# Kernel tuning notes

Hardware: AMD Instinct MI355X
Metric: run time of the kernel (lower is better)

The kernel has to match this reference:

```python
import jax, jax.numpy as jnp
import numpy as np

N_NODES = 25000
N_EDGES = 400000
D_FEAT = 64      # 2 * per-endpoint feature dim (concat of both endpoints)
STATE_DIM = 16
OUT_DIM = 16
MAX_IT = 5
THRESHOLD = 0.01


def setup_inputs() -> dict:
    key = jax.random.key(0)
    ks = jax.random.split(key, 8)
    edge_src = jax.random.randint(ks[0], (N_EDGES,), 0, N_NODES)
    edge_dst = jax.random.randint(ks[1], (N_EDGES,), 0, N_NODES)
    edge_feat = jax.random.normal(ks[2], (N_EDGES, D_FEAT), jnp.float32)
    w = lambda k, s: jax.random.normal(k, s, jnp.float32) * 0.1
    return {
        "edge_feat": edge_feat,
        "Wst1": w(ks[3], (D_FEAT + STATE_DIM, 2 * STATE_DIM)),
        "bst1": jnp.zeros((2 * STATE_DIM,), jnp.float32),
        "Wst2": w(ks[4], (2 * STATE_DIM, STATE_DIM)),
        "bst2": jnp.zeros((STATE_DIM,), jnp.float32),
        "Wout1": w(ks[5], (STATE_DIM, 2 * STATE_DIM)),
        "bout1": jnp.zeros((2 * STATE_DIM,), jnp.float32),
        "Wout2": w(ks[6], (2 * STATE_DIM, OUT_DIM)),
        "bout2": jnp.zeros((OUT_DIM,), jnp.float32),
        "edge_src": edge_src,
        "edge_dst": edge_dst,
        "n_nodes": N_NODES,
    }


def reference(edge_feat, Wst1, bst1, Wst2, bst2, Wout1, bout1, Wout2, bout2,
              edge_src, edge_dst, n_nodes):
    s = Wst2.shape[1]
    state0 = jnp.zeros((n_nodes, s), edge_feat.dtype)

    def step(carry, _):
        state, done = carry
        gat = state[edge_dst]                                   # [E, s] gather
        x = jnp.concatenate([edge_feat, gat], axis=1)           # [E, 2d+s]
        res = jnp.tanh(jnp.tanh(x @ Wst1 + bst1) @ Wst2 + bst2)  # state MLP
        new_state = jax.ops.segment_sum(res, edge_src, num_segments=n_nodes)
        # per-node L2 change; stop (freeze) once all nodes are below threshold
        dist = jnp.sqrt(jnp.sum((new_state - state) ** 2, axis=1) + 1e-10)
        converged = jnp.all(dist <= THRESHOLD)
        state = jnp.where(done, state, new_state)
        return (state, done | converged), None

    (state, _), _ = jax.lax.scan(step, (state0, jnp.array(False)), None, length=MAX_IT)
    h = jnp.tanh(state @ Wout1 + bout1)
    out = jax.nn.softmax(h @ Wout2 + bout2, axis=-1)  # [n_nodes, out_dim]
    return out
```

## Files before the change

### kernel.cpp

```cpp
#include <hip/hip_runtime.h>
#include <cstddef>

#define D_FEAT 64
#define S_DIM 16
#define H_DIM 32
#define OUT_DIM 16
#define MAX_IT 5

typedef _Float16 half8 __attribute__((ext_vector_type(8)));

__device__ __forceinline__ float fast_tanh(float x) {
    float xc = fminf(fmaxf(x, -15.0f), 15.0f);
    float e = __expf(2.0f * xc);
    return (e - 1.0f) / (e + 1.0f);
}

__global__ __launch_bounds__(256)
void k_hist(const int* __restrict__ src, int* __restrict__ deg, int E) {
    int e = blockIdx.x * 256 + threadIdx.x;
    if (e < E) atomicAdd(&deg[src[e]], 1);
}

__global__ __launch_bounds__(1024)
void k_scan(const int* __restrict__ deg, int* __restrict__ cursor, int N) {
    __shared__ int wsum[16];
    __shared__ int carry;
    int lane = threadIdx.x & 63;
    int wid = threadIdx.x >> 6;
    if (threadIdx.x == 0) carry = 0;
    __syncthreads();
    for (int base = 0; base < N; base += 1024) {
        int i = base + (int)threadIdx.x;
        int v = (i < N) ? deg[i] : 0;
        int incl = v;
#pragma unroll
        for (int off = 1; off < 64; off <<= 1) {
            int t = __shfl_up(incl, off, 64);
            if (lane >= off) incl += t;
        }
        if (lane == 63) wsum[wid] = incl;
        __syncthreads();
        if (wid == 0) {
            int w = (lane < 16) ? wsum[lane] : 0;
            int wi = w;
#pragma unroll
            for (int off = 1; off < 16; off <<= 1) {
                int t = __shfl_up(wi, off, 64);
                if (lane >= off) wi += t;
            }
            if (lane < 16) wsum[lane] = wi - w;
        }
        __syncthreads();
        int excl = incl - v + wsum[wid] + carry;
        if (i < N) cursor[i] = excl;
        __syncthreads();
        if ((int)threadIdx.x == 1023) carry = excl + v;
        __syncthreads();
    }
}

__global__ __launch_bounds__(256)
void k_scatter(const int* __restrict__ src, const int* __restrict__ dst,
               int* __restrict__ cursor, int* __restrict__ pos,
               int* __restrict__ dstp, int* __restrict__ srcp, int E) {
    int e = blockIdx.x * 256 + threadIdx.x;
    if (e >= E) return;
    int s = src[e];
    int p = atomicAdd(&cursor[s], 1);
    pos[e] = p;
    dstp[p] = dst[e];
    srcp[p] = s;
}

__global__ __launch_bounds__(256)
void k_pre(const float* __restrict__ feat, const float* __restrict__ Wst1,
           const float* __restrict__ bst1, const int* __restrict__ pos,
           _Float16* __restrict__ pre, int E) {
    int e = blockIdx.x * 256 + threadIdx.x;
    if (e >= E) return;
    float acc[H_DIM];
#pragma unroll
    for (int j = 0; j < H_DIM; ++j) acc[j] = bst1[j];
    const float4* f4 = reinterpret_cast<const float4*>(feat + (size_t)e * D_FEAT);
#pragma unroll 4
    for (int k4 = 0; k4 < D_FEAT / 4; ++k4) {
        float4 v = f4[k4];
        const float* w = Wst1 + k4 * 4 * H_DIM;
#pragma unroll
        for (int j = 0; j < H_DIM; ++j) acc[j] = fmaf(v.x, w[j], acc[j]);
#pragma unroll
        for (int j = 0; j < H_DIM; ++j) acc[j] = fmaf(v.y, w[H_DIM + j], acc[j]);
#pragma unroll
        for (int j = 0; j < H_DIM; ++j) acc[j] = fmaf(v.z, w[2 * H_DIM + j], acc[j]);
#pragma unroll
        for (int j = 0; j < H_DIM; ++j) acc[j] = fmaf(v.w, w[3 * H_DIM + j], acc[j]);
    }
    int p = pos[e];
    half8* op = reinterpret_cast<half8*>(pre + (size_t)p * H_DIM);
#pragma unroll
    for (int j8 = 0; j8 < 4; ++j8) {
        half8 v;
#pragma unroll
        for (int k = 0; k < 8; ++k) v[k] = (_Float16)acc[j8 * 8 + k];
        op[j8] = v;
    }
}

__global__ __launch_bounds__(256)
void k_edge(const _Float16* __restrict__ pre, const float* __restrict__ nodeH,
            const int* __restrict__ dstp, const int* __restrict__ srcp,
            const float* __restrict__ Wst2, const float* __restrict__ bst2,
            float* __restrict__ new_state, const int* __restrict__ flags,
            int it, int E) {
#pragma unroll
    for (int j = 0; j < MAX_IT; ++j)
        if (j < it && flags[2 + j] == 0) return;
    __shared__ float sres[256][17];
    __shared__ int ssrc[256];
    __shared__ int send[256];
    __shared__ int segs[256];
    __shared__ int wf[4];
    __shared__ int nseg;
    const int t = threadIdx.x;
    const int lane = t & 63;
    const int wid = t >> 6;
    const int base = blockIdx.x * 256;
    const int ep = base + t;
    const bool valid = ep < E;
    if (t == 0) nseg = 0;

    int s = valid ? srcp[ep] : (int)0x80000000;
    ssrc[t] = s;

    if (valid) {
        int d = dstp[ep];
        const half8* pp = reinterpret_cast<const half8*>(pre + (size_t)ep * H_DIM);
        const float4* hp = reinterpret_cast<const float4*>(nodeH + (size_t)d * H_DIM);
        float h[H_DIM];
#pragma unroll
        for (int j8 = 0; j8 < 4; ++j8) {
            half8 pv = pp[j8];
            float4 a = hp[j8 * 2], b = hp[j8 * 2 + 1];
            h[j8 * 8 + 0] = fast_tanh((float)pv[0] + a.x);
            h[j8 * 8 + 1] = fast_tanh((float)pv[1] + a.y);
            h[j8 * 8 + 2] = fast_tanh((float)pv[2] + a.z);
            h[j8 * 8 + 3] = fast_tanh((float)pv[3] + a.w);
            h[j8 * 8 + 4] = fast_tanh((float)pv[4] + b.x);
            h[j8 * 8 + 5] = fast_tanh((float)pv[5] + b.y);
            h[j8 * 8 + 6] = fast_tanh((float)pv[6] + b.z);
            h[j8 * 8 + 7] = fast_tanh((float)pv[7] + b.w);
        }
        float r[S_DIM];
#pragma unroll
        for (int i = 0; i < S_DIM; ++i) r[i] = bst2[i];
#pragma unroll
        for (int j = 0; j < H_DIM; ++j) {
            const float* w = Wst2 + (size_t)j * S_DIM;
            float hj = h[j];
#pragma unroll
            for (int i = 0; i < S_DIM; ++i) r[i] = fmaf(hj, w[i], r[i]);
        }
#pragma unroll
        for (int i = 0; i < S_DIM; ++i) sres[t][i] = fast_tanh(r[i]);
    }
    __syncthreads();

    bool head = (t == 0) || (ssrc[t - 1] != s);
    bool tail = (t == 255) || (ssrc[t + 1] != s);

    int mn = tail ? (t + 1) : 0x7fffffff;
#pragma unroll
    for (int off = 1; off < 64; off <<= 1) {
        int u = __shfl_down(mn, off, 64);
        if (lane + off < 64) mn = min(mn, u);
    }
    if (lane == 0) wf[wid] = mn;
    __syncthreads();
    int carry = 0x7fffffff;
#pragma unroll
    for (int w = 0; w < 4; ++w)
        if (w > wid) carry = min(carry, wf[w]);
    send[t] = min(mn, carry);
    int spos = -1;
    if (head && valid) spos = atomicAdd(&nseg, 1);
    if (spos >= 0) segs[spos] = t;
    __syncthreads();

    int ns = nseg;
    for (int w = t; w < ns * 16; w += 256) {
        int st = segs[w >> 4];
        int dim = w & 15;
        int en = send[st];
        int node = ssrc[st];
        float a = 0.f;
        for (int i = st; i < en; ++i) a += sres[i][dim];
        bool tS = (st > 0) || (base == 0) || (srcp[base - 1] != node);
        int gen = base + en;
        bool tE = (en < 256) || (gen >= E) || (srcp[gen] != node);
        float* p = new_state + (size_t)node * S_DIM + dim;
        if (tS && tE) *p = a;
        else atomicAdd(p, a);
    }
}

__global__ __launch_bounds__(256)
void k_node(float* __restrict__ state, float* __restrict__ new_state,
            float* __restrict__ nodeH, const float* __restrict__ Wst1,
            int* __restrict__ flags, int it, int N) {
#pragma unroll
    for (int j = 0; j < MAX_IT; ++j)
        if (j < it && flags[2 + j] == 0) return;
    int tt = blockIdx.x * 256 + threadIdx.x;
    int n = tt >> 2;
    int q = tt & 3;
    if (n >= N) return;
    float4* nsp = reinterpret_cast<float4*>(new_state + (size_t)n * S_DIM);
    float4* sp = reinterpret_cast<float4*>(state + (size_t)n * S_DIM);
    float4 acc = nsp[q];
    float4 old = sp[q];
    float dx = acc.x - old.x, dy = acc.y - old.y, dz = acc.z - old.z, dw = acc.w - old.w;
    float d2 = dx * dx + dy * dy + dz * dz + dw * dw;
    sp[q] = acc;
    nsp[q] = make_float4(0.f, 0.f, 0.f, 0.f);
    d2 += __shfl_xor(d2, 1);
    d2 += __shfl_xor(d2, 2);
    if (q == 0 && d2 + 1e-10f > 1e-4f) flags[2 + it] = 1;

    float st[S_DIM];
    st[q * 4 + 0] = acc.x; st[q * 4 + 1] = acc.y; st[q * 4 + 2] = acc.z; st[q * 4 + 3] = acc.w;
#pragma unroll
    for (int m = 1; m < 4; ++m) {
        int qs = q ^ m;
        st[qs * 4 + 0] = __shfl_xor(acc.x, m);
        st[qs * 4 + 1] = __shfl_xor(acc.y, m);
        st[qs * 4 + 2] = __shfl_xor(acc.z, m);
        st[qs * 4 + 3] = __shfl_xor(acc.w, m);
    }
    float hh[8];
#pragma unroll
    for (int j = 0; j < 8; ++j) hh[j] = 0.f;
#pragma unroll
    for (int k = 0; k < S_DIM; ++k) {
        const float* w = Wst1 + (size_t)(D_FEAT + k) * H_DIM + q * 8;
        float sk = st[k];
#pragma unroll
        for (int j = 0; j < 8; ++j) hh[j] = fmaf(sk, w[j], hh[j]);
    }
    float4* hp = reinterpret_cast<float4*>(nodeH + (size_t)n * H_DIM + q * 8);
    hp[0] = make_float4(hh[0], hh[1], hh[2], hh[3]);
    hp[1] = make_float4(hh[4], hh[5], hh[6], hh[7]);
}

__global__ __launch_bounds__(256)
void gnn_out(const float* __restrict__ state, const float* __restrict__ Wout1,
             const float* __restrict__ bout1, const float* __restrict__ Wout2,
             const float* __restrict__ bout2, float* __restrict__ out, int N) {
    int n = blockIdx.x * 256 + threadIdx.x;
    if (n >= N) return;
    float st[S_DIM];
    const float4* sp = reinterpret_cast<const float4*>(state + (size_t)n * S_DIM);
    float4 v0 = sp[0], v1 = sp[1], v2 = sp[2], v3 = sp[3];
    st[0] = v0.x; st[1] = v0.y; st[2] = v0.z; st[3] = v0.w;
    st[4] = v1.x; st[5] = v1.y; st[6] = v1.z; st[7] = v1.w;
    st[8] = v2.x; st[9] = v2.y; st[10] = v2.z; st[11] = v2.w;
    st[12] = v3.x; st[13] = v3.y; st[14] = v3.z; st[15] = v3.w;

    float h[H_DIM];
#pragma unroll
    for (int j = 0; j < H_DIM; ++j) {
        float acc = bout1[j];
#pragma unroll
        for (int k = 0; k < S_DIM; ++k) acc = fmaf(st[k], Wout1[(size_t)k * H_DIM + j], acc);
        h[j] = fast_tanh(acc);
    }
    float l[OUT_DIM];
#pragma unroll
    for (int i = 0; i < OUT_DIM; ++i) l[i] = bout2[i];
#pragma unroll
    for (int j = 0; j < H_DIM; ++j) {
        float hj = h[j];
#pragma unroll
        for (int i = 0; i < OUT_DIM; ++i) l[i] = fmaf(hj, Wout2[(size_t)j * OUT_DIM + i], l[i]);
    }
    float m = l[0];
#pragma unroll
    for (int i = 1; i < OUT_DIM; ++i) m = fmaxf(m, l[i]);
    float sum = 0.0f;
#pragma unroll
    for (int i = 0; i < OUT_DIM; ++i) {
        float tv = __expf(l[i] - m);
        l[i] = tv;
        sum += tv;
    }
    float inv = 1.0f / sum;
    float4* op = reinterpret_cast<float4*>(out + (size_t)n * OUT_DIM);
    op[0] = make_float4(l[0] * inv, l[1] * inv, l[2] * inv, l[3] * inv);
    op[1] = make_float4(l[4] * inv, l[5] * inv, l[6] * inv, l[7] * inv);
    op[2] = make_float4(l[8] * inv, l[9] * inv, l[10] * inv, l[11] * inv);
    op[3] = make_float4(l[12] * inv, l[13] * inv, l[14] * inv, l[15] * inv);
}

extern "C" void kernel_launch(void* const* d_in, const int* in_sizes, int n_in,
                              void* d_out, int out_size, void* d_ws, size_t ws_size,
                              hipStream_t stream) {
    const float* edge_feat = (const float*)d_in[0];
    const float* Wst1 = (const float*)d_in[1];
    const float* bst1 = (const float*)d_in[2];
    const float* Wst2 = (const float*)d_in[3];
    const float* bst2 = (const float*)d_in[4];
    const float* Wout1 = (const float*)d_in[5];
    const float* bout1 = (const float*)d_in[6];
    const float* Wout2 = (const float*)d_in[7];
    const float* bout2 = (const float*)d_in[8];
    const int* esrc = (const int*)d_in[9];
    const int* edst = (const int*)d_in[10];
    const int E = in_sizes[9];
    const int N = out_size / OUT_DIM;
    float* out = (float*)d_out;

    float* state = (float*)d_ws;
    float* nodeH = state + (size_t)N * S_DIM;
    float* new_state = nodeH + (size_t)N * H_DIM;
    _Float16* pre = (_Float16*)(new_state + (size_t)N * S_DIM);
    int* pos = (int*)(pre + (size_t)E * H_DIM);
    int* dstp = pos + E;
    int* srcp = dstp + E;
    int* deg = srcp + E;
    int* cursor = deg + N;
    int* flags = cursor + N;

    hipMemsetAsync(state, 0, (size_t)N * (S_DIM + H_DIM + S_DIM) * sizeof(float), stream);
    hipMemsetAsync(deg, 0, (size_t)N * sizeof(int), stream);
    hipMemsetAsync(flags, 0, 8 * sizeof(int), stream);

    int ebl = (E + 255) / 256;
    int nbl = (N + 255) / 256;
    int rbl = (N * 4 + 255) / 256;

    k_hist<<<ebl, 256, 0, stream>>>(esrc, deg, E);
    k_scan<<<1, 1024, 0, stream>>>(deg, cursor, N);
    k_scatter<<<ebl, 256, 0, stream>>>(esrc, edst, cursor, pos, dstp, srcp, E);
    k_pre<<<ebl, 256, 0, stream>>>(edge_feat, Wst1, bst1, pos, pre, E);

    for (int it = 0; it < MAX_IT; ++it) {
        k_edge<<<ebl, 256, 0, stream>>>(pre, nodeH, dstp, srcp, Wst2, bst2,
                                        new_state, flags, it, E);
        k_node<<<rbl, 256, 0, stream>>>(state, new_state, nodeH, Wst1, flags, it, N);
    }
    gnn_out<<<nbl, 256, 0, stream>>>(state, Wout1, bout1, Wout2, bout2, out, N);
}
```

Measured before the change: 304.1 us.

## Split each edge's state MLP across four threads in k_edge

Result: slower. 394.9 us (+29.9%).

```diff
diff --git a/kernel.cpp b/kernel.cpp
--- a/kernel.cpp
+++ b/kernel.cpp
@@ -106,7 +106,7 @@
     }
 }
 
-__global__ __launch_bounds__(256)
+__global__ __launch_bounds__(1024)
 void k_edge(const _Float16* __restrict__ pre, const float* __restrict__ nodeH,
             const int* __restrict__ dstp, const int* __restrict__ srcp,
             const float* __restrict__ Wst2, const float* __restrict__ bst2,
@@ -115,82 +115,96 @@
 #pragma unroll
     for (int j = 0; j < MAX_IT; ++j)
         if (j < it && flags[2 + j] == 0) return;
-    __shared__ float sres[256][17];
+    __shared__ float sres[256][20];
     __shared__ int ssrc[256];
-    __shared__ int send[256];
+    __shared__ int send_[256];
     __shared__ int segs[256];
     __shared__ int wf[4];
     __shared__ int nseg;
     const int t = threadIdx.x;
-    const int lane = t & 63;
-    const int wid = t >> 6;
     const int base = blockIdx.x * 256;
-    const int ep = base + t;
-    const bool valid = ep < E;
+    const int ei = t >> 2;
+    const int q = t & 3;
+    const int edge = base + ei;
+    const bool valid = edge < E;
     if (t == 0) nseg = 0;
-
-    int s = valid ? srcp[ep] : (int)0x80000000;
-    ssrc[t] = s;
+    if (t < 256) {
+        int ee = base + t;
+        ssrc[t] = (ee < E) ? srcp[ee] : (int)0x80000000;
+    }
 
     if (valid) {
-        int d = dstp[ep];
-        const half8* pp = reinterpret_cast<const half8*>(pre + (size_t)ep * H_DIM);
-        const float4* hp = reinterpret_cast<const float4*>(nodeH + (size_t)d * H_DIM);
-        float h[H_DIM];
-#pragma unroll
-        for (int j8 = 0; j8 < 4; ++j8) {
-            half8 pv = pp[j8];
-            float4 a = hp[j8 * 2], b = hp[j8 * 2 + 1];
-            h[j8 * 8 + 0] = fast_tanh((float)pv[0] + a.x);
-            h[j8 * 8 + 1] = fast_tanh((float)pv[1] + a.y);
-            h[j8 * 8 + 2] = fast_tanh((float)pv[2] + a.z);
-            h[j8 * 8 + 3] = fast_tanh((float)pv[3] + a.w);
-            h[j8 * 8 + 4] = fast_tanh((float)pv[4] + b.x);
-            h[j8 * 8 + 5] = fast_tanh((float)pv[5] + b.y);
-            h[j8 * 8 + 6] = fast_tanh((float)pv[6] + b.z);
-            h[j8 * 8 + 7] = fast_tanh((float)pv[7] + b.w);
+        int d = dstp[edge];
+        half8 pv = *reinterpret_cast<const half8*>(pre + (size_t)edge * H_DIM + q * 8);
+        const float4* hp = reinterpret_cast<const float4*>(nodeH + (size_t)d * H_DIM + q * 8);
+        float4 a = hp[0], b = hp[1];
+        float h8[8];
+        h8[0] = fast_tanh((float)pv[0] + a.x);
+        h8[1] = fast_tanh((float)pv[1] + a.y);
+        h8[2] = fast_tanh((float)pv[2] + a.z);
+        h8[3] = fast_tanh((float)pv[3] + a.w);
+        h8[4] = fast_tanh((float)pv[4] + b.x);
+        h8[5] = fast_tanh((float)pv[5] + b.y);
+        h8[6] = fast_tanh((float)pv[6] + b.z);
+        h8[7] = fast_tanh((float)pv[7] + b.w);
+
+        const int lq = (t & 63) & ~3;
+        float h_all[H_DIM];
+#pragma unroll
+        for (int j = 0; j < H_DIM; ++j)
+            h_all[j] = __shfl(h8[j & 7], lq + (j >> 3), 64);
+
+        const float4* W4 = reinterpret_cast<const float4*>(Wst2);
+        float4 bv = reinterpret_cast<const float4*>(bst2)[q];
+        float r0 = bv.x, r1 = bv.y, r2 = bv.z, r3 = bv.w;
+#pragma unroll
+        for (int j = 0; j < H_DIM; ++j) {
+            float hj = h_all[j];
+            float4 w = W4[j * 4 + q];
+            r0 = fmaf(hj, w.x, r0);
+            r1 = fmaf(hj, w.y, r1);
+            r2 = fmaf(hj, w.z, r2);
+            r3 = fmaf(hj, w.w, r3);
         }
-        float r[S_DIM];
-#pragma unroll
-        for (int i = 0; i < S_DIM; ++i) r[i] = bst2[i];
-#pragma unroll
-        for (int j = 0; j < H_DIM; ++j) {
-            const float* w = Wst2 + (size_t)j * S_DIM;
-            float hj = h[j];
-#pragma unroll
-            for (int i = 0; i < S_DIM; ++i) r[i] = fmaf(hj, w[i], r[i]);
+        float4 o = make_float4(fast_tanh(r0), fast_tanh(r1), fast_tanh(r2), fast_tanh(r3));
+        *reinterpret_cast<float4*>(&sres[ei][4 * q]) = o;
+    }
+    __syncthreads();
+
+    int s = 0, mn = 0x7fffffff;
+    bool head = false;
+    if (t < 256) {
+        s = ssrc[t];
+        head = (t == 0) || (ssrc[t - 1] != s);
+        bool tail = (t == 255) || (ssrc[t + 1] != s);
+        mn = tail ? (t + 1) : 0x7fffffff;
+        int lane = t & 63;
+#pragma unroll
+        for (int off = 1; off < 64; off <<= 1) {
+            int u = __shfl_down(mn, off, 64);
+            if (lane + off < 64) mn = min(mn, u);
         }
-#pragma unroll
-        for (int i = 0; i < S_DIM; ++i) sres[t][i] = fast_tanh(r[i]);
+        if (lane == 0) wf[t >> 6] = mn;
     }
     __syncthreads();
-
-    bool head = (t == 0) || (ssrc[t - 1] != s);
-    bool tail = (t == 255) || (ssrc[t + 1] != s);
-
-    int mn = tail ? (t + 1) : 0x7fffffff;
-#pragma unroll
-    for (int off = 1; off < 64; off <<= 1) {
-        int u = __shfl_down(mn, off, 64);
-        if (lane + off < 64) mn = min(mn, u);
-    }
-    if (lane == 0) wf[wid] = mn;
+    if (t < 256) {
+        int wid = t >> 6;
+        int carry = 0x7fffffff;
+#pragma unroll
+        for (int w = 0; w < 4; ++w)
+            if (w > wid) carry = min(carry, wf[w]);
+        send_[t] = min(mn, carry);
+        int spos = -1;
+        if (head && (base + t) < E) spos = atomicAdd(&nseg, 1);
+        if (spos >= 0) segs[spos] = t;
+    }
     __syncthreads();
-    int carry = 0x7fffffff;
-#pragma unroll
-    for (int w = 0; w < 4; ++w)
-        if (w > wid) carry = min(carry, wf[w]);
-    send[t] = min(mn, carry);
-    int spos = -1;
-    if (head && valid) spos = atomicAdd(&nseg, 1);
-    if (spos >= 0) segs[spos] = t;
-    __syncthreads();
 
     int ns = nseg;
-    for (int w = t; w < ns * 16; w += 256) {
+    for (int w = t; w < ns * 16; w += 1024) {
         int st = segs[w >> 4];
         int dim = w & 15;
-        int en = send[st];
+        int en = send_[st];
         int node = ssrc[st];
         float a = 0.f;
         for (int i = st; i < en; ++i) a += sres[i][dim];
@@ -343,8 +357,8 @@
     k_pre<<<ebl, 256, 0, stream>>>(edge_feat, Wst1, bst1, pos, pre, E);
 
     for (int it = 0; it < MAX_IT; ++it) {
-        k_edge<<<ebl, 256, 0, stream>>>(pre, nodeH, dstp, srcp, Wst2, bst2,
-                                        new_state, flags, it, E);
+        k_edge<<<ebl, 1024, 0, stream>>>(pre, nodeH, dstp, srcp, Wst2, bst2,
+                                         new_state, flags, it, E);
         k_node<<<rbl, 256, 0, stream>>>(state, new_state, nodeH, Wst1, flags, it, N);
     }
     gnn_out<<<nbl, 256, 0, stream>>>(state, Wout1, bout1, Wout2, bout2, out, N);
```

## Store node hidden projections in fp16, skip gather on first iteration, use row ends

Applied to the files above, without the earlier changes.

Measured after the change: 287.4 us. 1.06x faster.

```diff
diff --git a/kernel.cpp b/kernel.cpp
--- a/kernel.cpp
+++ b/kernel.cpp
@@ -82,7 +82,7 @@
 #pragma unroll
     for (int j = 0; j < H_DIM; ++j) acc[j] = bst1[j];
     const float4* f4 = reinterpret_cast<const float4*>(feat + (size_t)e * D_FEAT);
-#pragma unroll 4
+#pragma unroll 8
     for (int k4 = 0; k4 < D_FEAT / 4; ++k4) {
         float4 v = f4[k4];
         const float* w = Wst1 + k4 * 4 * H_DIM;
@@ -107,23 +107,22 @@
 }
 
 __global__ __launch_bounds__(256)
-void k_edge(const _Float16* __restrict__ pre, const float* __restrict__ nodeH,
+void k_edge(const _Float16* __restrict__ pre, const _Float16* __restrict__ nodeH16,
             const int* __restrict__ dstp, const int* __restrict__ srcp,
-            const float* __restrict__ Wst2, const float* __restrict__ bst2,
-            float* __restrict__ new_state, const int* __restrict__ flags,
-            int it, int E) {
+            const int* __restrict__ rowend, const float* __restrict__ Wst2,
+            const float* __restrict__ bst2, float* __restrict__ new_state,
+            const int* __restrict__ flags, int it, int E) {
 #pragma unroll
     for (int j = 0; j < MAX_IT; ++j)
         if (j < it && flags[2 + j] == 0) return;
     __shared__ float sres[256][17];
     __shared__ int ssrc[256];
-    __shared__ int send[256];
-    __shared__ int segs[256];
-    __shared__ int wf[4];
+    __shared__ int segnode[256];
+    __shared__ int segstart[256];
+    __shared__ int segend[256];
+    __shared__ int segflag[256];
     __shared__ int nseg;
     const int t = threadIdx.x;
-    const int lane = t & 63;
-    const int wid = t >> 6;
     const int base = blockIdx.x * 256;
     const int ep = base + t;
     const bool valid = ep < E;
@@ -133,22 +132,28 @@
     ssrc[t] = s;
 
     if (valid) {
-        int d = dstp[ep];
         const half8* pp = reinterpret_cast<const half8*>(pre + (size_t)ep * H_DIM);
-        const float4* hp = reinterpret_cast<const float4*>(nodeH + (size_t)d * H_DIM);
+        half8 p0 = pp[0], p1 = pp[1], p2 = pp[2], p3 = pp[3];
         float h[H_DIM];
-#pragma unroll
-        for (int j8 = 0; j8 < 4; ++j8) {
-            half8 pv = pp[j8];
-            float4 a = hp[j8 * 2], b = hp[j8 * 2 + 1];
-            h[j8 * 8 + 0] = fast_tanh((float)pv[0] + a.x);
-            h[j8 * 8 + 1] = fast_tanh((float)pv[1] + a.y);
-            h[j8 * 8 + 2] = fast_tanh((float)pv[2] + a.z);
-            h[j8 * 8 + 3] = fast_tanh((float)pv[3] + a.w);
-            h[j8 * 8 + 4] = fast_tanh((float)pv[4] + b.x);
-            h[j8 * 8 + 5] = fast_tanh((float)pv[5] + b.y);
-            h[j8 * 8 + 6] = fast_tanh((float)pv[6] + b.z);
-            h[j8 * 8 + 7] = fast_tanh((float)pv[7] + b.w);
+        if (it == 0) {
+#pragma unroll
+            for (int k = 0; k < 8; ++k) {
+                h[k]      = fast_tanh((float)p0[k]);
+                h[8 + k]  = fast_tanh((float)p1[k]);
+                h[16 + k] = fast_tanh((float)p2[k]);
+                h[24 + k] = fast_tanh((float)p3[k]);
+            }
+        } else {
+            int d = dstp[ep];
+            const half8* np = reinterpret_cast<const half8*>(nodeH16 + (size_t)d * H_DIM);
+            half8 n0 = np[0], n1 = np[1], n2 = np[2], n3 = np[3];
+#pragma unroll
+            for (int k = 0; k < 8; ++k) {
+                h[k]      = fast_tanh((float)p0[k] + (float)n0[k]);
+                h[8 + k]  = fast_tanh((float)p1[k] + (float)n1[k]);
+                h[16 + k] = fast_tanh((float)p2[k] + (float)n2[k]);
+                h[24 + k] = fast_tanh((float)p3[k] + (float)n3[k]);
+            }
         }
         float r[S_DIM];
 #pragma unroll
@@ -165,47 +170,38 @@
     }
     __syncthreads();
 
-    bool head = (t == 0) || (ssrc[t - 1] != s);
-    bool tail = (t == 255) || (ssrc[t + 1] != s);
-
-    int mn = tail ? (t + 1) : 0x7fffffff;
-#pragma unroll
-    for (int off = 1; off < 64; off <<= 1) {
-        int u = __shfl_down(mn, off, 64);
-        if (lane + off < 64) mn = min(mn, u);
-    }
-    if (lane == 0) wf[wid] = mn;
-    __syncthreads();
-    int carry = 0x7fffffff;
-#pragma unroll
-    for (int w = 0; w < 4; ++w)
-        if (w > wid) carry = min(carry, wf[w]);
-    send[t] = min(mn, carry);
-    int spos = -1;
-    if (head && valid) spos = atomicAdd(&nseg, 1);
-    if (spos >= 0) segs[spos] = t;
+    bool head = valid && ((t == 0) || (ssrc[t - 1] != s));
+    if (head) {
+        int slot = atomicAdd(&nseg, 1);
+        int re = rowend[s];
+        int en = re - base; if (en > 256) en = 256;
+        bool tS = (t > 0) || (ep == 0) || (srcp[ep - 1] != s);
+        bool tE = (re <= base + 256);
+        segnode[slot] = s;
+        segstart[slot] = t;
+        segend[slot] = en;
+        segflag[slot] = (tS && tE) ? 1 : 0;
+    }
     __syncthreads();
 
     int ns = nseg;
     for (int w = t; w < ns * 16; w += 256) {
-        int st = segs[w >> 4];
+        int slot = w >> 4;
         int dim = w & 15;
-        int en = send[st];
-        int node = ssrc[st];
+        int st = segstart[slot];
+        int en = segend[slot];
+        int node = segnode[slot];
         float a = 0.f;
         for (int i = st; i < en; ++i) a += sres[i][dim];
-        bool tS = (st > 0) || (base == 0) || (srcp[base - 1] != node);
-        int gen = base + en;
-        bool tE = (en < 256) || (gen >= E) || (srcp[gen] != node);
         float* p = new_state + (size_t)node * S_DIM + dim;
-        if (tS && tE) *p = a;
+        if (segflag[slot]) *p = a;
         else atomicAdd(p, a);
     }
 }
 
 __global__ __launch_bounds__(256)
 void k_node(float* __restrict__ state, float* __restrict__ new_state,
-            float* __restrict__ nodeH, const float* __restrict__ Wst1,
+            _Float16* __restrict__ nodeH16, const float* __restrict__ Wst1,
             int* __restrict__ flags, int it, int N) {
 #pragma unroll
     for (int j = 0; j < MAX_IT; ++j)
@@ -246,9 +242,10 @@
 #pragma unroll
         for (int j = 0; j < 8; ++j) hh[j] = fmaf(sk, w[j], hh[j]);
     }
-    float4* hp = reinterpret_cast<float4*>(nodeH + (size_t)n * H_DIM + q * 8);
-    hp[0] = make_float4(hh[0], hh[1], hh[2], hh[3]);
-    hp[1] = make_float4(hh[4], hh[5], hh[6], hh[7]);
+    half8 hv;
+#pragma unroll
+    for (int j = 0; j < 8; ++j) hv[j] = (_Float16)hh[j];
+    *reinterpret_cast<half8*>(nodeH16 + (size_t)n * H_DIM + q * 8) = hv;
 }
 
 __global__ __launch_bounds__(256)
@@ -319,17 +316,17 @@
     float* out = (float*)d_out;
 
     float* state = (float*)d_ws;
-    float* nodeH = state + (size_t)N * S_DIM;
-    float* new_state = nodeH + (size_t)N * H_DIM;
+    float* new_state = state + (size_t)N * S_DIM;
     _Float16* pre = (_Float16*)(new_state + (size_t)N * S_DIM);
-    int* pos = (int*)(pre + (size_t)E * H_DIM);
+    _Float16* nodeH16 = pre + (size_t)E * H_DIM;
+    int* pos = (int*)(nodeH16 + (size_t)N * H_DIM);
     int* dstp = pos + E;
     int* srcp = dstp + E;
     int* deg = srcp + E;
     int* cursor = deg + N;
     int* flags = cursor + N;
 
-    hipMemsetAsync(state, 0, (size_t)N * (S_DIM + H_DIM + S_DIM) * sizeof(float), stream);
+    hipMemsetAsync(state, 0, (size_t)N * S_DIM * 2 * sizeof(float), stream);
     hipMemsetAsync(deg, 0, (size_t)N * sizeof(int), stream);
     hipMemsetAsync(flags, 0, 8 * sizeof(int), stream);
 
@@ -343,9 +340,9 @@
     k_pre<<<ebl, 256, 0, stream>>>(edge_feat, Wst1, bst1, pos, pre, E);
 
     for (int it = 0; it < MAX_IT; ++it) {
-        k_edge<<<ebl, 256, 0, stream>>>(pre, nodeH, dstp, srcp, Wst2, bst2,
+        k_edge<<<ebl, 256, 0, stream>>>(pre, nodeH16, dstp, srcp, cursor, Wst2, bst2,
                                         new_state, flags, it, E);
-        k_node<<<rbl, 256, 0, stream>>>(state, new_state, nodeH, Wst1, flags, it, N);
+        k_node<<<rbl, 256, 0, stream>>>(state, new_state, nodeH16, Wst1, flags, it, N);
     }
     gnn_out<<<nbl, 256, 0, stream>>>(state, Wout1, bout1, Wout2, bout2, out, N);
 }
```
